# Kernel optimization log

Measured on AMD Instinct MI355X. Metric: run time of the kernel, lower is better.

The kernel has to match this reference:

```python
import jax, jax.numpy as jnp
import numpy as np

DIM_Q = 512
DIM_K = 512
DIM_V = 512
NUM_HEADS = 8
LN_EPS = 1e-5


def setup_inputs() -> dict:
    key = jax.random.key(0)
    ks = jax.random.split(key, 12)
    s_q = 1.0 / np.sqrt(DIM_Q)
    s_k = 1.0 / np.sqrt(DIM_K)
    s_v = 1.0 / np.sqrt(DIM_V)
    return {
        "Q": jax.random.normal(ks[0], (8, 1024, DIM_Q), dtype=jnp.float32),
        "K": jax.random.normal(ks[1], (8, 1024, DIM_K), dtype=jnp.float32),
        "Wq": jax.random.uniform(ks[2], (DIM_Q, DIM_V), jnp.float32, -s_q, s_q),
        "bq": jax.random.uniform(ks[3], (DIM_V,), jnp.float32, -s_q, s_q),
        "Wk": jax.random.uniform(ks[4], (DIM_K, DIM_V), jnp.float32, -s_k, s_k),
        "bk": jax.random.uniform(ks[5], (DIM_V,), jnp.float32, -s_k, s_k),
        "Wv": jax.random.uniform(ks[6], (DIM_K, DIM_V), jnp.float32, -s_k, s_k),
        "bv": jax.random.uniform(ks[7], (DIM_V,), jnp.float32, -s_k, s_k),
        "Wo": jax.random.uniform(ks[8], (DIM_V, DIM_V), jnp.float32, -s_v, s_v),
        "bo": jax.random.uniform(ks[9], (DIM_V,), jnp.float32, -s_v, s_v),
        "g0": jnp.ones((DIM_V,), jnp.float32),
        "b0": jnp.zeros((DIM_V,), jnp.float32),
        "g1": jnp.ones((DIM_V,), jnp.float32),
        "b1": jnp.zeros((DIM_V,), jnp.float32),
    }


def _layer_norm(x, gamma, beta):
    mu = jnp.mean(x, axis=-1, keepdims=True)
    var = jnp.var(x, axis=-1, keepdims=True)
    return (x - mu) * jax.lax.rsqrt(var + LN_EPS) * gamma + beta


def reference(Q, K, Wq, bq, Wk, bk, Wv, bv, Wo, bo, g0, b0, g1, b1):
    B, Nq, _ = Q.shape
    Nk = K.shape[1]
    H = NUM_HEADS
    d = DIM_V // H  # head dim

    Qp = Q @ Wq + bq                      # [B, Nq, dim_V]
    Kp = K @ Wk + bk                      # [B, Nk, dim_V]
    Vp = K @ Wv + bv                      # [B, Nk, dim_V]

    Qh = Qp.reshape(B, Nq, H, d)
    Kh = Kp.reshape(B, Nk, H, d)
    Vh = Vp.reshape(B, Nk, H, d)

    scores = jnp.einsum("bqhd,bkhd->bhqk", Qh, Kh) / jnp.sqrt(jnp.float32(d))
    A = jax.nn.softmax(scores, axis=-1)   # [B, H, Nq, Nk]
    Oh = jnp.einsum("bhqk,bkhd->bqhd", A, Vh) + Qh  # residual with projected Q
    O = Oh.reshape(B, Nq, DIM_V)

    O = _layer_norm(O, g0, b0)
    O = O + jax.nn.relu(O @ Wo + bo)
    O = _layer_norm(O, g1, b1)
    return O
```

## Files before the change

### kernel.cpp

```cpp
#include <hip/hip_runtime.h>
#include <math.h>

#define DV 512
#define HD 64
#define NHEADS 8
#define SEQ 1024
#define NBATCH 8
#define MROWS (NBATCH * SEQ)

typedef __bf16 bf16;
typedef __bf16 bf16x8 __attribute__((ext_vector_type(8)));
typedef __bf16 bf16x4 __attribute__((ext_vector_type(4)));
typedef float f32x4 __attribute__((ext_vector_type(4)));

__device__ inline void gload_lds16(const void* g, void* l) {
  __builtin_amdgcn_global_load_lds(
      (const __attribute__((address_space(1))) unsigned int*)g,
      (__attribute__((address_space(3))) unsigned int*)l, 16, 0, 0);
}

__device__ __forceinline__ bf16x8 cvt8(float4 a, float4 b) {
  bf16x8 o;
  o[0] = (bf16)a.x; o[1] = (bf16)a.y; o[2] = (bf16)a.z; o[3] = (bf16)a.w;
  o[4] = (bf16)b.x; o[5] = (bf16)b.y; o[6] = (bf16)b.z; o[7] = (bf16)b.w;
  return o;
}

__global__ __launch_bounds__(256) void prep_w(
    const float* __restrict__ W0, const float* __restrict__ W1,
    const float* __restrict__ W2, const float* __restrict__ W3,
    bf16* __restrict__ T0, bf16* __restrict__ T1,
    bf16* __restrict__ T2, bf16* __restrict__ T3)
{
  const int z = blockIdx.z;
  const float* W = z == 0 ? W0 : z == 1 ? W1 : z == 2 ? W2 : W3;
  bf16* WT = z == 0 ? T0 : z == 1 ? T1 : z == 2 ? T2 : T3;
  __shared__ float T[64][65];
  const int t = threadIdx.x;
  const int k0 = (blockIdx.x >> 3) * 64, n0 = (blockIdx.x & 7) * 64;
#pragma unroll
  for (int p = 0; p < 4; ++p) {
    int r = p * 16 + (t >> 4), c = (t & 15) * 4;
    float4 v = *(const float4*)&W[(size_t)(k0 + r) * DV + n0 + c];
    T[r][c] = v.x; T[r][c + 1] = v.y; T[r][c + 2] = v.z; T[r][c + 3] = v.w;
  }
  __syncthreads();
#pragma unroll
  for (int p = 0; p < 2; ++p) {
    int n = p * 32 + (t >> 3), kc = (t & 7) * 8;
    bf16x8 o;
#pragma unroll
    for (int j = 0; j < 8; ++j) o[j] = (bf16)T[kc + j][n];
    *(bf16x8*)&WT[(size_t)(n0 + n) * DV + k0 + kc] = o;
  }
}

template<bool SA>
__device__ __forceinline__ void proj_core(
    const float* __restrict__ Sg, const bf16* __restrict__ Wg,
    int s0, int w0, bf16* Ss, f32x4 (*acc)[4])
{
  const int tid = threadIdx.x;
  const int lane = tid & 63, w = tid >> 6;
  const int wm = w >> 1, wn = w & 1;
  const int cl = lane & 15, qd = lane >> 4;
  const int sw = SA ? wm : wn;
  const int ww = SA ? wn : wm;

  size_t offS[4];
  int sOff[4];
#pragma unroll
  for (int t = 0; t < 4; ++t) {
    int S = t * 256 + tid;
    int row = S >> 3, kq = (S & 7) ^ (row & 7);
    offS[t] = (size_t)(s0 + row) * DV + kq * 8;
    sOff[t] = S * 8;
  }

  const bf16* Wp[4];
#pragma unroll
  for (int i = 0; i < 4; ++i)
    Wp[i] = Wg + (size_t)(w0 + ww * 64 + i * 16 + cl) * DV + qd * 8;

  float4 r0[4], r1[4];
#pragma unroll
  for (int t = 0; t < 4; ++t) {
    r0[t] = *(const float4*)(Sg + offS[t]);
    r1[t] = *(const float4*)(Sg + offS[t] + 4);
  }
#pragma unroll
  for (int t = 0; t < 4; ++t) *(bf16x8*)(Ss + sOff[t]) = cvt8(r0[t], r1[t]);

  bf16x8 wcur[4][2], wnext[4][2];
#pragma unroll
  for (int i = 0; i < 4; ++i)
#pragma unroll
    for (int cc = 0; cc < 2; ++cc)
      wcur[i][cc] = *(const bf16x8*)(Wp[i] + cc * 32);

  for (int it = 0; it < 8; ++it) {
    __syncthreads();
    const int cur = it & 1;
    const int nb = (cur ^ 1) * 8192;
    const bool has = (it + 1 < 8);
    if (has) {
      const size_t kn = (size_t)(it + 1) * 64;
#pragma unroll
      for (int t = 0; t < 4; ++t) {
        r0[t] = *(const float4*)(Sg + kn + offS[t]);
        r1[t] = *(const float4*)(Sg + kn + offS[t] + 4);
      }
#pragma unroll
      for (int i = 0; i < 4; ++i)
#pragma unroll
        for (int cc = 0; cc < 2; ++cc)
          wnext[i][cc] = *(const bf16x8*)(Wp[i] + kn + cc * 32);
    }
    const bf16* S_ = Ss + cur * 8192;
#pragma unroll
    for (int cc = 0; cc < 2; ++cc) {
      bf16x8 sf[4];
#pragma unroll
      for (int j = 0; j < 4; ++j) {
        int row = sw * 64 + j * 16 + cl;
        int slot = row * 8 + ((cc * 4 + qd) ^ (row & 7));
        sf[j] = *(const bf16x8*)(S_ + (size_t)slot * 8);
      }
#pragma unroll
      for (int mi = 0; mi < 4; ++mi)
#pragma unroll
        for (int ni = 0; ni < 4; ++ni) {
          if (SA)
            acc[mi][ni] = __builtin_amdgcn_mfma_f32_16x16x32_bf16(
                sf[mi], wcur[ni][cc], acc[mi][ni], 0, 0, 0);
          else
            acc[mi][ni] = __builtin_amdgcn_mfma_f32_16x16x32_bf16(
                wcur[mi][cc], sf[ni], acc[mi][ni], 0, 0, 0);
        }
    }
    if (has) {
#pragma unroll
      for (int t = 0; t < 4; ++t)
        *(bf16x8*)(Ss + nb + sOff[t]) = cvt8(r0[t], r1[t]);
#pragma unroll
      for (int i = 0; i < 4; ++i)
#pragma unroll
        for (int cc = 0; cc < 2; ++cc) wcur[i][cc] = wnext[i][cc];
    }
  }
}

__global__ __launch_bounds__(256) void gemm_proj(
    const float* __restrict__ Qf, const float* __restrict__ Kf,
    const bf16* __restrict__ WqT, const bf16* __restrict__ WkT,
    const bf16* __restrict__ WvT,
    const float* __restrict__ bq, const float* __restrict__ bk,
    const float* __restrict__ bv,
    bf16* __restrict__ Qp, bf16* __restrict__ Kp, bf16* __restrict__ VpT)
{
  __shared__ bf16 Ss[2 * 8192];
  const int z = blockIdx.z;
  int m0, n0, N;
  f32x4 acc[4][4] = {};
  if (z < 2) {
    m0 = (blockIdx.x & 63) * 128; n0 = (blockIdx.x >> 6) * 128; N = DV;
    proj_core<true>(z ? Kf : Qf, z ? WkT : WqT, m0, n0, Ss, acc);
  } else {
    n0 = (blockIdx.x & 63) * 128; m0 = (blockIdx.x >> 6) * 128; N = MROWS;
    proj_core<false>(Kf, WvT, n0, m0, Ss, acc);
  }

  const float* bias = z == 0 ? bq : z == 1 ? bk : bv;
  bf16* C = z == 0 ? Qp : z == 1 ? Kp : VpT;
  const int lane = threadIdx.x & 63, w = threadIdx.x >> 6;
  const int wm = w >> 1, wn = w & 1;
  const int cl = lane & 15, qd = lane >> 4;
  float bcol[4] = {0.f, 0.f, 0.f, 0.f};
  if (z < 2)
#pragma unroll
    for (int ni = 0; ni < 4; ++ni) bcol[ni] = bias[n0 + wn * 64 + ni * 16 + cl];
#pragma unroll
  for (int mi = 0; mi < 4; ++mi)
#pragma unroll
    for (int r = 0; r < 4; ++r) {
      int gm = m0 + wm * 64 + mi * 16 + qd * 4 + r;
      float brow = (z == 2) ? bias[gm] : 0.f;
#pragma unroll
      for (int ni = 0; ni < 4; ++ni) {
        int gn = n0 + wn * 64 + ni * 16 + cl;
        float v = acc[mi][ni][r] + (z == 2 ? brow : bcol[ni]);
        C[(size_t)gm * N + gn] = (bf16)v;
      }
    }
}

__global__ __launch_bounds__(256) void attn_mfma(
    const bf16* __restrict__ Qp, const bf16* __restrict__ Kp,
    const bf16* __restrict__ VpT, bf16* __restrict__ Orb)
{
  __shared__ bf16 Ks[2][64 * 64];
  __shared__ bf16 Vs[2][64 * 64];
  __shared__ bf16 Ps[4][32 * 72];

  const int tid = threadIdx.x, lane = tid & 63, w = tid >> 6;
  const int cl = lane & 15, qd = lane >> 4;
  const int bh = blockIdx.x, b = bh >> 3, h = bh & 7;
  const int q0w = blockIdx.y * 128 + w * 32;

  const float SCL = 0.18033688011112042f;
  bf16x8 qa[2][2];
#pragma unroll
  for (int qt = 0; qt < 2; ++qt)
#pragma unroll
    for (int ch = 0; ch < 2; ++ch) {
      bf16x8 v = *(const bf16x8*)(Qp + ((size_t)b * SEQ + q0w + qt * 16 + cl) * DV
                                  + h * HD + ch * 32 + qd * 8);
#pragma unroll
      for (int j = 0; j < 8; ++j) v[j] = (bf16)((float)v[j] * SCL);
      qa[qt][ch] = v;
    }

  f32x4 o[4][2] = {};
  float lrun[2] = {0.f, 0.f};

  const bf16* Kbase = Kp + (size_t)b * SEQ * DV + h * HD;
  const bf16* Vbase = VpT + (size_t)h * HD * MROWS + (size_t)b * SEQ;
  bf16* Pw = &Ps[w][0];

  const int Sa = tid, Sb = 256 + tid;
  const int kRowA = Sa >> 3, kDgA = (Sa & 7) ^ (kRowA & 7);
  const int kRowB = Sb >> 3, kDgB = (Sb & 7) ^ (kRowB & 7);
  const size_t kOffA = (size_t)kRowA * DV + kDgA * 8;
  const size_t kOffB = (size_t)kRowB * DV + kDgB * 8;
  const size_t vOffA = (size_t)kRowA * MROWS + kDgA * 8;
  const size_t vOffB = (size_t)kRowB * MROWS + kDgB * 8;

  gload_lds16(Kbase + kOffA, &Ks[0][(size_t)(w * 64) * 8]);
  gload_lds16(Kbase + kOffB, &Ks[0][(size_t)(256 + w * 64) * 8]);
  gload_lds16(Vbase + vOffA, &Vs[0][(size_t)(w * 64) * 8]);
  gload_lds16(Vbase + vOffB, &Vs[0][(size_t)(256 + w * 64) * 8]);

  for (int it = 0; it < SEQ / 64; ++it) {
    __syncthreads();
    const int cur = it & 1;
    if (it + 1 < SEQ / 64) {
      const size_t kt = (size_t)(it + 1) * 64;
      gload_lds16(Kbase + kt * DV + kOffA, &Ks[cur ^ 1][(size_t)(w * 64) * 8]);
      gload_lds16(Kbase + kt * DV + kOffB, &Ks[cur ^ 1][(size_t)(256 + w * 64) * 8]);
      gload_lds16(Vbase + kt + vOffA, &Vs[cur ^ 1][(size_t)(w * 64) * 8]);
      gload_lds16(Vbase + kt + vOffB, &Vs[cur ^ 1][(size_t)(256 + w * 64) * 8]);
    }
    const bf16* K_ = &Ks[cur][0];
    const bf16* V_ = &Vs[cur][0];

    f32x4 sc[4][2] = {};
#pragma unroll
    for (int ch = 0; ch < 2; ++ch) {
      bf16x8 kf[4];
#pragma unroll
      for (int kt4 = 0; kt4 < 4; ++kt4) {
        int key = kt4 * 16 + cl;
        int slot = key * 8 + ((ch * 4 + qd) ^ (key & 7));
        kf[kt4] = *(const bf16x8*)(K_ + (size_t)slot * 8);
      }
#pragma unroll
      for (int kt4 = 0; kt4 < 4; ++kt4)
#pragma unroll
        for (int qt = 0; qt < 2; ++qt)
          sc[kt4][qt] = __builtin_amdgcn_mfma_f32_16x16x32_bf16(
              kf[kt4], qa[qt][ch], sc[kt4][qt], 0, 0, 0);
    }

#pragma unroll
    for (int qt = 0; qt < 2; ++qt) {
      float sum = 0.f;
#pragma unroll
      for (int kt4 = 0; kt4 < 4; ++kt4) {
        float p0 = __builtin_amdgcn_exp2f(sc[kt4][qt][0]);
        float p1 = __builtin_amdgcn_exp2f(sc[kt4][qt][1]);
        float p2 = __builtin_amdgcn_exp2f(sc[kt4][qt][2]);
        float p3 = __builtin_amdgcn_exp2f(sc[kt4][qt][3]);
        sum += (p0 + p1) + (p2 + p3);
        bf16x4 pk;
        pk[0] = (bf16)p0; pk[1] = (bf16)p1; pk[2] = (bf16)p2; pk[3] = (bf16)p3;
        *(bf16x4*)(Pw + (size_t)(qt * 16 + cl) * 72 + kt4 * 16 + qd * 4) = pk;
      }
      sum += __shfl_xor(sum, 16);
      sum += __shfl_xor(sum, 32);
      lrun[qt] += sum;
    }

#pragma unroll
    for (int kc = 0; kc < 2; ++kc) {
      bf16x8 pb[2];
#pragma unroll
      for (int qt = 0; qt < 2; ++qt)
        pb[qt] = *(const bf16x8*)(Pw + (size_t)(qt * 16 + cl) * 72 + kc * 32 + qd * 8);
#pragma unroll
      for (int dt = 0; dt < 4; ++dt) {
        int d = dt * 16 + cl;
        int slot = d * 8 + ((kc * 4 + qd) ^ (d & 7));
        bf16x8 vf = *(const bf16x8*)(V_ + (size_t)slot * 8);
#pragma unroll
        for (int qt = 0; qt < 2; ++qt)
          o[dt][qt] = __builtin_amdgcn_mfma_f32_16x16x32_bf16(
              vf, pb[qt], o[dt][qt], 0, 0, 0);
      }
    }
  }

#pragma unroll
  for (int qt = 0; qt < 2; ++qt) {
    float inv = 1.f / lrun[qt];
    size_t rowoff = ((size_t)b * SEQ + q0w + qt * 16 + cl) * DV + h * HD;
#pragma unroll
    for (int dt = 0; dt < 4; ++dt) {
      bf16x4 rv = *(const bf16x4*)(Qp + rowoff + dt * 16 + qd * 4);
      bf16x4 st;
      st[0] = (bf16)(o[dt][qt][0] * inv + (float)rv[0]);
      st[1] = (bf16)(o[dt][qt][1] * inv + (float)rv[1]);
      st[2] = (bf16)(o[dt][qt][2] * inv + (float)rv[2]);
      st[3] = (bf16)(o[dt][qt][3] * inv + (float)rv[3]);
      *(bf16x4*)(Orb + rowoff + dt * 16 + qd * 4) = st;
    }
  }
}

__global__ __launch_bounds__(256) void gemm_fused(
    const bf16* __restrict__ Orb, const bf16* __restrict__ WoT,
    const float* __restrict__ bo,
    const float* __restrict__ g0, const float* __restrict__ b0,
    const float* __restrict__ g1, const float* __restrict__ b1,
    float* __restrict__ out)
{
  __shared__ bf16 Bsm[32 * 512];
  __shared__ bf16 As[2][2048 * 8];
  const int tid = threadIdx.x, lane = tid & 63, w = tid >> 6;
  const int cl = lane & 15, qd = lane >> 4;
  const int m0 = blockIdx.x * 32;

  size_t offA[8];
  int uOff[8];
#pragma unroll
  for (int t = 0; t < 8; ++t) {
    int S = t * 256 + tid;
    int frow = S >> 2, kq = (S & 3) ^ ((frow >> 1) & 3);
    offA[t] = (size_t)frow * DV + kq * 8;
    uOff[t] = (t * 256 + w * 64) * 8;
  }

#pragma unroll
  for (int t = 0; t < 8; ++t)
    gload_lds16(WoT + offA[t], As[0] + uOff[t]);

  {
    const int q = tid >> 3, c0 = (tid & 7) * 64;
    const bf16* src = Orb + (size_t)(m0 + q) * DV + c0;
    float x[64];
    float s = 0.f, s2 = 0.f;
#pragma unroll
    for (int j = 0; j < 8; ++j) {
      bf16x8 xv = *(const bf16x8*)(src + j * 8);
#pragma unroll
      for (int e = 0; e < 8; ++e) {
        float f = (float)xv[e];
        x[j * 8 + e] = f; s += f; s2 += f * f;
      }
    }
    s  += __shfl_xor(s, 1);  s  += __shfl_xor(s, 2);  s  += __shfl_xor(s, 4);
    s2 += __shfl_xor(s2, 1); s2 += __shfl_xor(s2, 2); s2 += __shfl_xor(s2, 4);
    float mu = s * (1.f / DV);
    float inv = rsqrtf(s2 * (1.f / DV) - mu * mu + 1e-5f);
#pragma unroll
    for (int j = 0; j < 8; ++j) {
      float4 ga = *(const float4*)(g0 + c0 + j * 8);
      float4 gb = *(const float4*)(g0 + c0 + j * 8 + 4);
      float4 ba = *(const float4*)(b0 + c0 + j * 8);
      float4 bb = *(const float4*)(b0 + c0 + j * 8 + 4);
      bf16x8 o;
      o[0] = (bf16)((x[j*8+0] - mu) * inv * ga.x + ba.x);
      o[1] = (bf16)((x[j*8+1] - mu) * inv * ga.y + ba.y);
      o[2] = (bf16)((x[j*8+2] - mu) * inv * ga.z + ba.z);
      o[3] = (bf16)((x[j*8+3] - mu) * inv * ga.w + ba.w);
      o[4] = (bf16)((x[j*8+4] - mu) * inv * gb.x + bb.x);
      o[5] = (bf16)((x[j*8+5] - mu) * inv * gb.y + bb.y);
      o[6] = (bf16)((x[j*8+6] - mu) * inv * gb.z + bb.z);
      o[7] = (bf16)((x[j*8+7] - mu) * inv * gb.w + bb.w);
      int g = (tid & 7) * 8 + j;
      int slot = q * 64 + (g ^ (q & 7));
      *(bf16x8*)(Bsm + (size_t)slot * 8) = o;
    }
  }

  f32x4 acc[8][2] = {};
  for (int it = 0; it < 16; ++it) {
    __syncthreads();
    const int cur = it & 1;
    if (it + 1 < 16) {
#pragma unroll
      for (int t = 0; t < 8; ++t)
        gload_lds16(WoT + (size_t)(it + 1) * 32 + offA[t], As[cur ^ 1] + uOff[t]);
    }
    bf16x8 bfr[2];
#pragma unroll
    for (int nt = 0; nt < 2; ++nt) {
      int q = nt * 16 + cl;
      int slot = q * 64 + ((it * 4 + qd) ^ (q & 7));
      bfr[nt] = *(const bf16x8*)(Bsm + (size_t)slot * 8);
    }
#pragma unroll
    for (int mt = 0; mt < 8; ++mt) {
      int frow = (w * 8 + mt) * 16 + cl;
      int slot = frow * 4 + (qd ^ ((frow >> 1) & 3));
      bf16x8 af = *(const bf16x8*)(As[cur] + (size_t)slot * 8);
#pragma unroll
      for (int nt = 0; nt < 2; ++nt)
        acc[mt][nt] = __builtin_amdgcn_mfma_f32_16x16x32_bf16(
            af, bfr[nt], acc[mt][nt], 0, 0, 0);
    }
  }

  __syncthreads();
  float* red = (float*)As;
  float y[8][2][4];
  float sy[2], sy2[2];
#pragma unroll
  for (int nt = 0; nt < 2; ++nt) {
    sy[nt] = 0.f; sy2[nt] = 0.f;
    const int q = nt * 16 + cl;
#pragma unroll
    for (int mt = 0; mt < 8; ++mt) {
      const int f0 = (w * 8 + mt) * 16 + qd * 4;
      float4 bov = *(const float4*)(bo + f0);
      int g = f0 >> 3;
      int slot = q * 64 + (g ^ (q & 7));
      bf16x4 rv = *(const bf16x4*)(Bsm + (size_t)slot * 8 + (qd & 1) * 4);
      const float* bp = (const float*)&bov;
#pragma unroll
      for (int r = 0; r < 4; ++r) {
        float v = fmaxf(acc[mt][nt][r] + bp[r], 0.f) + (float)rv[r];
        y[mt][nt][r] = v;
        sy[nt] += v; sy2[nt] += v * v;
      }
    }
    sy[nt]  += __shfl_xor(sy[nt], 16);  sy[nt]  += __shfl_xor(sy[nt], 32);
    sy2[nt] += __shfl_xor(sy2[nt], 16); sy2[nt] += __shfl_xor(sy2[nt], 32);
  }
  if (qd == 0) {
#pragma unroll
    for (int nt = 0; nt < 2; ++nt) {
      int q = nt * 16 + cl;
      red[(q * 4 + w) * 2 + 0] = sy[nt];
      red[(q * 4 + w) * 2 + 1] = sy2[nt];
    }
  }
  __syncthreads();
#pragma unroll
  for (int nt = 0; nt < 2; ++nt) {
    const int q = nt * 16 + cl;
    float s = 0.f, s2 = 0.f;
#pragma unroll
    for (int ww = 0; ww < 4; ++ww) {
      s  += red[(q * 4 + ww) * 2 + 0];
      s2 += red[(q * 4 + ww) * 2 + 1];
    }
    float mu1 = s * (1.f / DV);
    float inv1 = rsqrtf(s2 * (1.f / DV) - mu1 * mu1 + 1e-5f);
    size_t rowoff = (size_t)(m0 + q) * DV;
#pragma unroll
    for (int mt = 0; mt < 8; ++mt) {
      const int f0 = (w * 8 + mt) * 16 + qd * 4;
      float4 gv = *(const float4*)(g1 + f0);
      float4 bv = *(const float4*)(b1 + f0);
      float4 ov;
      ov.x = (y[mt][nt][0] - mu1) * inv1 * gv.x + bv.x;
      ov.y = (y[mt][nt][1] - mu1) * inv1 * gv.y + bv.y;
      ov.z = (y[mt][nt][2] - mu1) * inv1 * gv.z + bv.z;
      ov.w = (y[mt][nt][3] - mu1) * inv1 * gv.w + bv.w;
      *(float4*)(out + rowoff + f0) = ov;
    }
  }
}

extern "C" void kernel_launch(void* const* d_in, const int* in_sizes, int n_in,
                              void* d_out, int out_size, void* d_ws, size_t ws_size,
                              hipStream_t stream)
{
  const float* Q  = (const float*)d_in[0];
  const float* Kf = (const float*)d_in[1];
  const float* Wq = (const float*)d_in[2];
  const float* bq = (const float*)d_in[3];
  const float* Wk = (const float*)d_in[4];
  const float* bk = (const float*)d_in[5];
  const float* Wv = (const float*)d_in[6];
  const float* bv = (const float*)d_in[7];
  const float* Wo = (const float*)d_in[8];
  const float* bo = (const float*)d_in[9];
  const float* g0 = (const float*)d_in[10];
  const float* b0 = (const float*)d_in[11];
  const float* g1 = (const float*)d_in[12];
  const float* b1 = (const float*)d_in[13];
  float* out = (float*)d_out;

  const size_t MB = 1ull << 20;
  char* W = (char*)d_ws;
  bf16* Orb = (bf16*)(W + 0);
  bf16* Qp  = (bf16*)(W + 8 * MB);
  bf16* Kp  = (bf16*)(W + 16 * MB);
  bf16* VpT = (bf16*)(W + 24 * MB);
  bf16* WqT = (bf16*)(W + 32 * MB);
  bf16* WkT = (bf16*)(W + 32 * MB + 512 * 1024);
  bf16* WvT = (bf16*)(W + 33 * MB);
  bf16* WoT = (bf16*)(W + 33 * MB + 512 * 1024);

  dim3 blk(256);
  prep_w<<<dim3(64, 1, 4), blk, 0, stream>>>(Wq, Wk, Wv, Wo, WqT, WkT, WvT, WoT);
  gemm_proj<<<dim3(256, 1, 3), blk, 0, stream>>>(
      Q, Kf, WqT, WkT, WvT, bq, bk, bv, Qp, Kp, VpT);
  attn_mfma<<<dim3(NBATCH * NHEADS, SEQ / 128), blk, 0, stream>>>(Qp, Kp, VpT, Orb);
  gemm_fused<<<dim3(MROWS / 32), blk, 0, stream>>>(
      Orb, WoT, bo, g0, b0, g1, b1, out);
}
```

Baseline: 192.7 us.

## Stream fp32 activations and bf16 weights via direct global-to-LDS loads in projection GEMM

Result: faster. 188.8 us (-2.0%).

```diff
diff --git a/kernel.cpp b/kernel.cpp
--- a/kernel.cpp
+++ b/kernel.cpp
@@ -58,7 +58,7 @@
 template<bool SA>
 __device__ __forceinline__ void proj_core(
     const float* __restrict__ Sg, const bf16* __restrict__ Wg,
-    int s0, int w0, bf16* Ss, f32x4 (*acc)[4])
+    int s0, int w0, float* Sf, bf16* Wb, f32x4 (*acc)[4])
 {
   const int tid = threadIdx.x;
   const int lane = tid & 63, w = tid >> 6;
@@ -67,86 +67,70 @@
   const int sw = SA ? wm : wn;
   const int ww = SA ? wn : wm;
 
-  size_t offS[4];
-  int sOff[4];
+  size_t offS[4]; int uS[4];
 #pragma unroll
   for (int t = 0; t < 4; ++t) {
     int S = t * 256 + tid;
-    int row = S >> 3, kq = (S & 7) ^ (row & 7);
-    offS[t] = (size_t)(s0 + row) * DV + kq * 8;
-    sOff[t] = S * 8;
-  }
-
-  const bf16* Wp[4];
-#pragma unroll
-  for (int i = 0; i < 4; ++i)
-    Wp[i] = Wg + (size_t)(w0 + ww * 64 + i * 16 + cl) * DV + qd * 8;
-
-  float4 r0[4], r1[4];
-#pragma unroll
-  for (int t = 0; t < 4; ++t) {
-    r0[t] = *(const float4*)(Sg + offS[t]);
-    r1[t] = *(const float4*)(Sg + offS[t] + 4);
-  }
-#pragma unroll
-  for (int t = 0; t < 4; ++t) *(bf16x8*)(Ss + sOff[t]) = cvt8(r0[t], r1[t]);
-
-  bf16x8 wcur[4][2], wnext[4][2];
-#pragma unroll
-  for (int i = 0; i < 4; ++i)
-#pragma unroll
-    for (int cc = 0; cc < 2; ++cc)
-      wcur[i][cc] = *(const bf16x8*)(Wp[i] + cc * 32);
-
-  for (int it = 0; it < 8; ++it) {
+    int row = S >> 3, g = (S & 7) ^ (row & 7);
+    offS[t] = (size_t)(s0 + row) * DV + g * 4;
+    uS[t] = (t * 256 + w * 64) * 4;
+  }
+  size_t offW[2]; int uW[2];
+#pragma unroll
+  for (int t = 0; t < 2; ++t) {
+    int S = t * 256 + tid;
+    int row = S >> 2, g = (S & 3) ^ ((row >> 1) & 3);
+    offW[t] = (size_t)(w0 + row) * DV + g * 8;
+    uW[t] = (t * 256 + w * 64) * 8;
+  }
+
+#pragma unroll
+  for (int t = 0; t < 4; ++t) gload_lds16(Sg + offS[t], Sf + uS[t]);
+#pragma unroll
+  for (int t = 0; t < 2; ++t) gload_lds16(Wg + offW[t], Wb + uW[t]);
+
+  for (int it = 0; it < 16; ++it) {
     __syncthreads();
     const int cur = it & 1;
-    const int nb = (cur ^ 1) * 8192;
-    const bool has = (it + 1 < 8);
-    if (has) {
-      const size_t kn = (size_t)(it + 1) * 64;
-#pragma unroll
-      for (int t = 0; t < 4; ++t) {
-        r0[t] = *(const float4*)(Sg + kn + offS[t]);
-        r1[t] = *(const float4*)(Sg + kn + offS[t] + 4);
-      }
-#pragma unroll
-      for (int i = 0; i < 4; ++i)
-#pragma unroll
-        for (int cc = 0; cc < 2; ++cc)
-          wnext[i][cc] = *(const bf16x8*)(Wp[i] + kn + cc * 32);
-    }
-    const bf16* S_ = Ss + cur * 8192;
-#pragma unroll
-    for (int cc = 0; cc < 2; ++cc) {
-      bf16x8 sf[4];
-#pragma unroll
-      for (int j = 0; j < 4; ++j) {
-        int row = sw * 64 + j * 16 + cl;
-        int slot = row * 8 + ((cc * 4 + qd) ^ (row & 7));
-        sf[j] = *(const bf16x8*)(S_ + (size_t)slot * 8);
-      }
-#pragma unroll
-      for (int mi = 0; mi < 4; ++mi)
-#pragma unroll
-        for (int ni = 0; ni < 4; ++ni) {
-          if (SA)
-            acc[mi][ni] = __builtin_amdgcn_mfma_f32_16x16x32_bf16(
-                sf[mi], wcur[ni][cc], acc[mi][ni], 0, 0, 0);
-          else
-            acc[mi][ni] = __builtin_amdgcn_mfma_f32_16x16x32_bf16(
-                wcur[mi][cc], sf[ni], acc[mi][ni], 0, 0, 0);
-        }
-    }
-    if (has) {
+    if (it + 1 < 16) {
+      const size_t kn = (size_t)(it + 1) * 32;
 #pragma unroll
       for (int t = 0; t < 4; ++t)
-        *(bf16x8*)(Ss + nb + sOff[t]) = cvt8(r0[t], r1[t]);
-#pragma unroll
-      for (int i = 0; i < 4; ++i)
-#pragma unroll
-        for (int cc = 0; cc < 2; ++cc) wcur[i][cc] = wnext[i][cc];
-    }
+        gload_lds16(Sg + kn + offS[t], Sf + (cur ^ 1) * 4096 + uS[t]);
+#pragma unroll
+      for (int t = 0; t < 2; ++t)
+        gload_lds16(Wg + kn + offW[t], Wb + (cur ^ 1) * 4096 + uW[t]);
+    }
+    const float* S_ = Sf + cur * 4096;
+    const bf16* W_ = Wb + cur * 4096;
+
+    bf16x8 sf[4], wf[4];
+#pragma unroll
+    for (int j = 0; j < 4; ++j) {
+      int row = sw * 64 + j * 16 + cl;
+      int lo = row * 8 + ((2 * qd) ^ (row & 7));
+      int hi = row * 8 + ((2 * qd + 1) ^ (row & 7));
+      float4 a = *(const float4*)(S_ + lo * 4);
+      float4 b = *(const float4*)(S_ + hi * 4);
+      sf[j] = cvt8(a, b);
+    }
+#pragma unroll
+    for (int j = 0; j < 4; ++j) {
+      int row = ww * 64 + j * 16 + cl;
+      int slot = row * 4 + (qd ^ ((row >> 1) & 3));
+      wf[j] = *(const bf16x8*)(W_ + (size_t)slot * 8);
+    }
+#pragma unroll
+    for (int mi = 0; mi < 4; ++mi)
+#pragma unroll
+      for (int ni = 0; ni < 4; ++ni) {
+        if (SA)
+          acc[mi][ni] = __builtin_amdgcn_mfma_f32_16x16x32_bf16(
+              sf[mi], wf[ni], acc[mi][ni], 0, 0, 0);
+        else
+          acc[mi][ni] = __builtin_amdgcn_mfma_f32_16x16x32_bf16(
+              wf[mi], sf[ni], acc[mi][ni], 0, 0, 0);
+      }
   }
 }
 
@@ -158,16 +142,17 @@
     const float* __restrict__ bv,
     bf16* __restrict__ Qp, bf16* __restrict__ Kp, bf16* __restrict__ VpT)
 {
-  __shared__ bf16 Ss[2 * 8192];
+  __shared__ float Sf[2 * 4096];
+  __shared__ bf16 Wb[2 * 4096];
   const int z = blockIdx.z;
   int m0, n0, N;
   f32x4 acc[4][4] = {};
   if (z < 2) {
     m0 = (blockIdx.x & 63) * 128; n0 = (blockIdx.x >> 6) * 128; N = DV;
-    proj_core<true>(z ? Kf : Qf, z ? WkT : WqT, m0, n0, Ss, acc);
+    proj_core<true>(z ? Kf : Qf, z ? WkT : WqT, m0, n0, Sf, Wb, acc);
   } else {
     n0 = (blockIdx.x & 63) * 128; m0 = (blockIdx.x >> 6) * 128; N = MROWS;
-    proj_core<false>(Kf, WvT, n0, m0, Ss, acc);
+    proj_core<false>(Kf, WvT, n0, m0, Sf, Wb, acc);
   }
 
   const float* bias = z == 0 ? bq : z == 1 ? bk : bv;
```
